# Kernel optimization log

Hardware: AMD Instinct MI355X
Metric: run time of the kernel (lower is better)

## Reference

```python
import jax, jax.numpy as jnp
import numpy as np

IN_DIM = 2048
OUT_DIM = 2048
BASIS_DIM = 64
BATCH = 4
SEQ = 4096
EPS = 1e-5


def _make_bbasis():
    k = np.arange(BASIS_DIM, dtype=np.float64)[:, None]  # (K,1)
    i = np.arange(OUT_DIM, dtype=np.float64)[None, :]    # (1,D)
    return jnp.asarray(np.cos(2.0 * np.pi * (k + 1.0) / (i + 2.0)), dtype=jnp.float32)


def setup_inputs() -> dict:
    key = jax.random.key(0)
    k1, k2, k3, k4 = jax.random.split(key, 4)
    x = jax.random.normal(k1, (BATCH, SEQ, IN_DIM), dtype=jnp.float32)
    # nn.init.uniform_(-0.1, 0.1) style scaling for weights
    W = jax.random.uniform(k2, (OUT_DIM, IN_DIM), dtype=jnp.float32, minval=-0.1, maxval=0.1)
    W_res = jax.random.uniform(k3, (OUT_DIM, IN_DIM), dtype=jnp.float32, minval=-0.1, maxval=0.1)
    Acoeff = jax.random.uniform(k4, (OUT_DIM, BASIS_DIM), dtype=jnp.float32, minval=-0.1, maxval=0.1)
    gamma = jnp.ones((OUT_DIM,), dtype=jnp.float32)
    beta = jnp.zeros((OUT_DIM,), dtype=jnp.float32)
    Bbasis = _make_bbasis()
    return {"x": x, "W": W, "W_res": W_res, "gamma": gamma, "beta": beta,
            "Acoeff": Acoeff, "Bbasis": Bbasis}


def reference(x, W, W_res, gamma, beta, Acoeff, Bbasis):
    # residual projection (use_residual == 'separate')
    residual = jnp.einsum('bsi,oi->bso', x, W_res)          # (B,S,D)
    transformed = jnp.einsum('bsi,oi->bso', x, W)           # (B,S,D)
    # LayerNorm over last dim
    mean = jnp.mean(transformed, axis=-1, keepdims=True)
    var = jnp.mean(jnp.square(transformed - mean), axis=-1, keepdims=True)
    normalized = (transformed - mean) * jax.lax.rsqrt(var + EPS) * gamma + beta
    # periodic basis gather
    seq_len = x.shape[1]
    j = jnp.arange(seq_len) % BASIS_DIM                      # (S,)
    B_vec = Bbasis[j]                                        # (S,D)
    A_vec = Acoeff[:, j].T                                   # (S,D)
    scalars = jnp.einsum('bsd,sd->bs', normalized, B_vec)    # (B,S)
    return scalars[:, :, None] * A_vec[None] + residual      # (B,S,D)
```

## Files before the change

### kernel.cpp

```cpp
#include <hip/hip_runtime.h>
#include <hip/hip_bf16.h>

#define KDIM   2048
#define DDIM   2048
#define MROWS  16384
#define BASIS  64
#define EPSLN  1e-5f
#define NKT    32

typedef __bf16 bf16x8 __attribute__((ext_vector_type(8)));
typedef float  f32x4  __attribute__((ext_vector_type(4)));
typedef unsigned short u16x8 __attribute__((ext_vector_type(8)));

static __device__ __forceinline__ unsigned short f2bf(float f) {
  union { float f; unsigned int u; } v; v.f = f;
  unsigned int r = v.u + 0x7FFFu + ((v.u >> 16) & 1u);
  return (unsigned short)(r >> 16);
}
static __device__ __forceinline__ float bf2f(unsigned short h) {
  union { unsigned int u; float f; } v; v.u = ((unsigned int)h) << 16;
  return v.f;
}

__global__ __launch_bounds__(256) void prep(
    const float* __restrict__ x, const float* __restrict__ W,
    const float* __restrict__ Wres, const float* __restrict__ Ac,
    unsigned short* __restrict__ xbf, unsigned short* __restrict__ Wc,
    float* __restrict__ At) {
  const int b = blockIdx.x, t = threadIdx.x;
  if (b < 2048) {
    const float4* in = (const float4*)x;
    ushort4* op = (ushort4*)xbf;
    const int base = b * 4096;
#pragma unroll
    for (int k = 0; k < 16; ++k) {
      const int i = base + k * 256 + t;
      float4 v = in[i];
      op[i] = make_ushort4(f2bf(v.x), f2bf(v.y), f2bf(v.z), f2bf(v.w));
    }
  } else if (b < 3072) {
    const bool isW = (b < 2560);
    const float4* in = (const float4*)(isW ? W : Wres);
    ushort4* op = (ushort4*)(Wc + (isW ? 0 : 4194304));
    const int base = (isW ? (b - 2048) : (b - 2560)) * 2048;
#pragma unroll
    for (int k = 0; k < 8; ++k) {
      const int i = base + k * 256 + t;
      float4 v = in[i];
      op[i] = make_ushort4(f2bf(v.x), f2bf(v.y), f2bf(v.z), f2bf(v.w));
    }
  } else {
    const int j = b - 3072;
    for (int d = t; d < DDIM; d += 256)
      At[j * DDIM + d] = Ac[d * BASIS + j];
  }
}

__device__ __forceinline__ void gload16(const void* g, void* l) {
  __builtin_amdgcn_global_load_lds(
      (const __attribute__((address_space(1))) unsigned int*)(unsigned long long)g,
      (__attribute__((address_space(3))) unsigned int*)(unsigned int)(unsigned long long)l,
      16, 0, 0);
}
__device__ __forceinline__ void bar() { asm volatile("s_barrier" ::: "memory"); }

__global__ __launch_bounds__(512, 2) void gemm_dual(
    const unsigned short* __restrict__ Abf,
    const unsigned short* __restrict__ Bbf,
    unsigned short* __restrict__ Tout,
    unsigned short* __restrict__ Rout)
{
  __shared__ __align__(16) unsigned short As[2 * 256 * 64];
  __shared__ __align__(16) unsigned short Bs[2 * 256 * 64];

  const int tid  = threadIdx.x;
  const int lane = tid & 63;
  const int wave = tid >> 6;

  const int bid = blockIdx.x;
  const int wg  = (bid & 7) * 128 + (bid >> 3);
  const int bm  = wg >> 4;
  const int bn  = wg & 15;
  const int brow0 = bm * 256;
  const int bcol0 = bn * 256;

  const int srow  = tid >> 3;
  const int sslot = (tid & 7) ^ (srow & 7);
  const unsigned short* pA = Abf + (size_t)(brow0 + srow) * KDIM + sslot * 8;
  const unsigned short* pB = Bbf + (size_t)(bcol0 + srow) * KDIM + sslot * 8;
  const int ldst = wave * 512;

  const int wm   = wave >> 2;
  const int wn   = wave & 3;
  const int frow = lane & 15;
  const int kgrp = lane >> 4;

#define SA(d, kk, c) gload16(pA + (size_t)(c)*64*KDIM + (kk)*64, As + (d)*16384 + (c)*4096 + ldst)
#define SB(d, kk, c) gload16(pB + (size_t)(c)*64*KDIM + (kk)*64, Bs + (d)*16384 + (c)*4096 + ldst)
#define RD_A(mf, kc) (*(const bf16x8*)(Ard + (wm*128 + (mf)*16 + frow)*64 + ((((kc)*4 + kgrp) ^ (frow & 7)) << 3)))
#define RD_B(j, kc)  (*(const bf16x8*)(Brd + (wn*64  + (j)*16  + frow)*64 + ((((kc)*4 + kgrp) ^ (frow & 7)) << 3)))

  f32x4 acc[8][4] = {};

  SA(0,0,0); SA(0,0,1); SA(0,0,2); SA(0,0,3);
  SB(0,0,0); SB(0,0,1); SB(0,0,2); SB(0,0,3);
  SB(1,1,0); SB(1,1,1);
  SA(1,1,0); SA(1,1,2);
  SB(1,1,2); SB(1,1,3);
  asm volatile("s_waitcnt vmcnt(6)" ::: "memory");
  __builtin_amdgcn_sched_barrier(0);
  bar();

  for (int kt = 0; kt < NKT; ++kt) {
    const int d = kt & 1;
    const unsigned short* Ard = As + d * 16384;
    const unsigned short* Brd = Bs + d * 16384;

    bf16x8 bv[4][2], af0[2], af1[2];

#pragma unroll
    for (int j = 0; j < 4; ++j) { bv[j][0] = RD_B(j, 0); bv[j][1] = RD_B(j, 1); }
    af0[0] = RD_A(0, 0); af0[1] = RD_A(0, 1);
    af1[0] = RD_A(1, 0); af1[1] = RD_A(1, 1);
    if (kt < NKT - 1) { SA(d ^ 1, kt + 1, 1); SA(d ^ 1, kt + 1, 3); }
    bar();
    __builtin_amdgcn_s_setprio(1);
#pragma unroll
    for (int j = 0; j < 4; ++j) {
      acc[0][j] = __builtin_amdgcn_mfma_f32_16x16x32_bf16(af0[0], bv[j][0], acc[0][j], 0, 0, 0);
      acc[0][j] = __builtin_amdgcn_mfma_f32_16x16x32_bf16(af0[1], bv[j][1], acc[0][j], 0, 0, 0);
      acc[1][j] = __builtin_amdgcn_mfma_f32_16x16x32_bf16(af1[0], bv[j][0], acc[1][j], 0, 0, 0);
      acc[1][j] = __builtin_amdgcn_mfma_f32_16x16x32_bf16(af1[1], bv[j][1], acc[1][j], 0, 0, 0);
    }
    __builtin_amdgcn_s_setprio(0);
    __builtin_amdgcn_sched_barrier(0);
    bar();

    af0[0] = RD_A(2, 0); af0[1] = RD_A(2, 1);
    af1[0] = RD_A(3, 0); af1[1] = RD_A(3, 1);
    if (kt < NKT - 2) { SB(d, kt + 2, 0); SB(d, kt + 2, 1); }
    bar();
    __builtin_amdgcn_s_setprio(1);
#pragma unroll
    for (int j = 0; j < 4; ++j) {
      acc[2][j] = __builtin_amdgcn_mfma_f32_16x16x32_bf16(af0[0], bv[j][0], acc[2][j], 0, 0, 0);
      acc[2][j] = __builtin_amdgcn_mfma_f32_16x16x32_bf16(af0[1], bv[j][1], acc[2][j], 0, 0, 0);
      acc[3][j] = __builtin_amdgcn_mfma_f32_16x16x32_bf16(af1[0], bv[j][0], acc[3][j], 0, 0, 0);
      acc[3][j] = __builtin_amdgcn_mfma_f32_16x16x32_bf16(af1[1], bv[j][1], acc[3][j], 0, 0, 0);
    }
    __builtin_amdgcn_s_setprio(0);
    __builtin_amdgcn_sched_barrier(0);
    bar();

    af0[0] = RD_A(4, 0); af0[1] = RD_A(4, 1);
    af1[0] = RD_A(5, 0); af1[1] = RD_A(5, 1);
    if (kt < NKT - 2) { SA(d, kt + 2, 0); SA(d, kt + 2, 2); }
    bar();
    __builtin_amdgcn_s_setprio(1);
#pragma unroll
    for (int j = 0; j < 4; ++j) {
      acc[4][j] = __builtin_amdgcn_mfma_f32_16x16x32_bf16(af0[0], bv[j][0], acc[4][j], 0, 0, 0);
      acc[4][j] = __builtin_amdgcn_mfma_f32_16x16x32_bf16(af0[1], bv[j][1], acc[4][j], 0, 0, 0);
      acc[5][j] = __builtin_amdgcn_mfma_f32_16x16x32_bf16(af1[0], bv[j][0], acc[5][j], 0, 0, 0);
      acc[5][j] = __builtin_amdgcn_mfma_f32_16x16x32_bf16(af1[1], bv[j][1], acc[5][j], 0, 0, 0);
    }
    __builtin_amdgcn_s_setprio(0);
    __builtin_amdgcn_sched_barrier(0);
    bar();

    af0[0] = RD_A(6, 0); af0[1] = RD_A(6, 1);
    af1[0] = RD_A(7, 0); af1[1] = RD_A(7, 1);
    if (kt < NKT - 2) { SB(d, kt + 2, 2); SB(d, kt + 2, 3); }
    bar();
    __builtin_amdgcn_s_setprio(1);
#pragma unroll
    for (int j = 0; j < 4; ++j) {
      acc[6][j] = __builtin_amdgcn_mfma_f32_16x16x32_bf16(af0[0], bv[j][0], acc[6][j], 0, 0, 0);
      acc[6][j] = __builtin_amdgcn_mfma_f32_16x16x32_bf16(af0[1], bv[j][1], acc[6][j], 0, 0, 0);
      acc[7][j] = __builtin_amdgcn_mfma_f32_16x16x32_bf16(af1[0], bv[j][0], acc[7][j], 0, 0, 0);
      acc[7][j] = __builtin_amdgcn_mfma_f32_16x16x32_bf16(af1[1], bv[j][1], acc[7][j], 0, 0, 0);
    }
    __builtin_amdgcn_s_setprio(0);
    if (kt < NKT - 2) { asm volatile("s_waitcnt vmcnt(6)" ::: "memory"); }
    else              { asm volatile("s_waitcnt vmcnt(0)" ::: "memory"); }
    __builtin_amdgcn_sched_barrier(0);
    bar();
  }

  unsigned short* Cb = (bn < 8) ? Tout : Rout;
  const int c0 = (bn < 8) ? bcol0 : (bcol0 - 2048);
#pragma unroll
  for (int i = 0; i < 8; ++i) {
    const int r0 = brow0 + wm * 128 + i * 16 + kgrp * 4;
#pragma unroll
    for (int j = 0; j < 4; ++j) {
      const int col = c0 + wn * 64 + j * 16 + frow;
#pragma unroll
      for (int r = 0; r < 4; ++r)
        Cb[(size_t)(r0 + r) * DDIM + col] = f2bf(acc[i][j][r]);
    }
  }
#undef SA
#undef SB
#undef RD_A
#undef RD_B
}

__global__ __launch_bounds__(256) void epilogue(
    const unsigned short* __restrict__ T, const unsigned short* __restrict__ R,
    const float* __restrict__ Bb, const float* __restrict__ At,
    const float* __restrict__ gam, const float* __restrict__ bet,
    float* __restrict__ out)
{
  __shared__ float red[16];
  const int row = blockIdx.x;
  const int s   = row & 4095;
  const int j   = s & 63;
  const int tid = threadIdx.x;
  const size_t rb = (size_t)row * DDIM;
  const int d0 = tid * 8;

  u16x8 tv = *(const u16x8*)(T + rb + d0);
  float t[8];
#pragma unroll
  for (int k = 0; k < 8; ++k) t[k] = bf2f(tv[k]);

  float sum = 0.f, sq = 0.f;
#pragma unroll
  for (int k = 0; k < 8; ++k) { sum += t[k]; sq += t[k] * t[k]; }
#pragma unroll
  for (int off = 32; off > 0; off >>= 1) {
    sum += __shfl_down(sum, off);
    sq  += __shfl_down(sq,  off);
  }
  if ((tid & 63) == 0) { red[tid >> 6] = sum; red[4 + (tid >> 6)] = sq; }
  __syncthreads();
  if (tid == 0) {
    float sAll = red[0] + red[1] + red[2] + red[3];
    float qAll = red[4] + red[5] + red[6] + red[7];
    float m = sAll * (1.0f / 2048.0f);
    float v = qAll * (1.0f / 2048.0f) - m * m;
    red[8] = m;
    red[9] = rsqrtf(v + EPSLN);
  }
  __syncthreads();
  const float mean = red[8], rstd = red[9];

  const size_t jb = (size_t)j * DDIM;
  float4 g0 = *(const float4*)(gam + d0), g1 = *(const float4*)(gam + d0 + 4);
  float4 b0 = *(const float4*)(bet + d0), b1 = *(const float4*)(bet + d0 + 4);
  float4 w0 = *(const float4*)(Bb + jb + d0), w1 = *(const float4*)(Bb + jb + d0 + 4);

  float sc =
      ((t[0] - mean) * rstd * g0.x + b0.x) * w0.x +
      ((t[1] - mean) * rstd * g0.y + b0.y) * w0.y +
      ((t[2] - mean) * rstd * g0.z + b0.z) * w0.z +
      ((t[3] - mean) * rstd * g0.w + b0.w) * w0.w +
      ((t[4] - mean) * rstd * g1.x + b1.x) * w1.x +
      ((t[5] - mean) * rstd * g1.y + b1.y) * w1.y +
      ((t[6] - mean) * rstd * g1.z + b1.z) * w1.z +
      ((t[7] - mean) * rstd * g1.w + b1.w) * w1.w;
#pragma unroll
  for (int off = 32; off > 0; off >>= 1) sc += __shfl_down(sc, off);
  if ((tid & 63) == 0) red[10 + (tid >> 6)] = sc;
  __syncthreads();
  const float scalar = red[10] + red[11] + red[12] + red[13];

  u16x8 rv = *(const u16x8*)(R + rb + d0);
  float4 a0 = *(const float4*)(At + jb + d0), a1 = *(const float4*)(At + jb + d0 + 4);
  float4 o0, o1;
  o0.x = scalar * a0.x + bf2f(rv[0]);  o0.y = scalar * a0.y + bf2f(rv[1]);
  o0.z = scalar * a0.z + bf2f(rv[2]);  o0.w = scalar * a0.w + bf2f(rv[3]);
  o1.x = scalar * a1.x + bf2f(rv[4]);  o1.y = scalar * a1.y + bf2f(rv[5]);
  o1.z = scalar * a1.z + bf2f(rv[6]);  o1.w = scalar * a1.w + bf2f(rv[7]);
  *(float4*)(out + rb + d0)     = o0;
  *(float4*)(out + rb + d0 + 4) = o1;
}

extern "C" void kernel_launch(void* const* d_in, const int* in_sizes, int n_in,
                              void* d_out, int out_size, void* d_ws, size_t ws_size,
                              hipStream_t stream) {
  const float* x      = (const float*)d_in[0];
  const float* W      = (const float*)d_in[1];
  const float* Wres   = (const float*)d_in[2];
  const float* gamma  = (const float*)d_in[3];
  const float* beta   = (const float*)d_in[4];
  const float* Acoeff = (const float*)d_in[5];
  const float* Bbasis = (const float*)d_in[6];
  float* out = (float*)d_out;
  char* ws = (char*)d_ws;

  unsigned short* xbf = (unsigned short*)ws;
  unsigned short* Wc  = (unsigned short*)(ws + 67108864);
  unsigned short* T   = (unsigned short*)(ws + 83886080);
  unsigned short* Rbf = (unsigned short*)(ws + 150994944);
  float* At           = (float*)(ws + 218103808);

  prep<<<3136, 256, 0, stream>>>(x, W, Wres, Acoeff, xbf, Wc, At);

  gemm_dual<<<1024, 512, 0, stream>>>(xbf, Wc, T, Rbf);

  epilogue<<<16384, 256, 0, stream>>>(T, Rbf, Bbasis, At, gamma, beta, out);
}
```

Measured before the change: 538.9 us.

## Restructure epilogue to one row per wave with folded LayerNorm algebra; add lgkm waits

The epilogue now assigns one basis index j per block and processes 16 rows sharing that j, two per wave. The per-column gamma*Bbasis products and their sums, plus the beta·Bbasis sum and the Acoeff row, are precomputed once in registers. Each row then needs a single pass computing sum, sum of squares and the dot product, reduced with wave shuffles only, with no LDS and no __syncthreads. The GEMM main loop also gets explicit lgkmcnt(0) waits before each MFMA cluster. These waits may serialize LDS reads with compute but make the scheduling explicit.

```diff
diff --git a/kernel.cpp b/kernel.cpp
--- a/kernel.cpp
+++ b/kernel.cpp
@@ -63,6 +63,8 @@
       16, 0, 0);
 }
 __device__ __forceinline__ void bar() { asm volatile("s_barrier" ::: "memory"); }
+#define LGKM0 do { asm volatile("s_waitcnt lgkmcnt(0)" ::: "memory"); \
+                   __builtin_amdgcn_sched_barrier(0); } while (0)
 
 __global__ __launch_bounds__(512, 2) void gemm_dual(
     const unsigned short* __restrict__ Abf,
@@ -124,6 +126,7 @@
     af1[0] = RD_A(1, 0); af1[1] = RD_A(1, 1);
     if (kt < NKT - 1) { SA(d ^ 1, kt + 1, 1); SA(d ^ 1, kt + 1, 3); }
     bar();
+    LGKM0;
     __builtin_amdgcn_s_setprio(1);
 #pragma unroll
     for (int j = 0; j < 4; ++j) {
@@ -140,6 +143,7 @@
     af1[0] = RD_A(3, 0); af1[1] = RD_A(3, 1);
     if (kt < NKT - 2) { SB(d, kt + 2, 0); SB(d, kt + 2, 1); }
     bar();
+    LGKM0;
     __builtin_amdgcn_s_setprio(1);
 #pragma unroll
     for (int j = 0; j < 4; ++j) {
@@ -156,6 +160,7 @@
     af1[0] = RD_A(5, 0); af1[1] = RD_A(5, 1);
     if (kt < NKT - 2) { SA(d, kt + 2, 0); SA(d, kt + 2, 2); }
     bar();
+    LGKM0;
     __builtin_amdgcn_s_setprio(1);
 #pragma unroll
     for (int j = 0; j < 4; ++j) {
@@ -172,6 +177,7 @@
     af1[0] = RD_A(7, 0); af1[1] = RD_A(7, 1);
     if (kt < NKT - 2) { SB(d, kt + 2, 2); SB(d, kt + 2, 3); }
     bar();
+    LGKM0;
     __builtin_amdgcn_s_setprio(1);
 #pragma unroll
     for (int j = 0; j < 4; ++j) {
@@ -206,75 +212,76 @@
 #undef RD_B
 }
 
-__global__ __launch_bounds__(256) void epilogue(
+__global__ __launch_bounds__(512) void epilogue(
     const unsigned short* __restrict__ T, const unsigned short* __restrict__ R,
     const float* __restrict__ Bb, const float* __restrict__ At,
     const float* __restrict__ gam, const float* __restrict__ bet,
     float* __restrict__ out)
 {
-  __shared__ float red[16];
-  const int row = blockIdx.x;
-  const int s   = row & 4095;
-  const int j   = s & 63;
-  const int tid = threadIdx.x;
-  const size_t rb = (size_t)row * DDIM;
-  const int d0 = tid * 8;
-
-  u16x8 tv = *(const u16x8*)(T + rb + d0);
-  float t[8];
-#pragma unroll
-  for (int k = 0; k < 8; ++k) t[k] = bf2f(tv[k]);
-
-  float sum = 0.f, sq = 0.f;
-#pragma unroll
-  for (int k = 0; k < 8; ++k) { sum += t[k]; sq += t[k] * t[k]; }
+  const int b   = blockIdx.x;
+  const int j   = b & 63;
+  const int seg = b >> 6;
+  const int wv  = threadIdx.x >> 6;
+  const int l   = threadIdx.x & 63;
+  const size_t jb = (size_t)j * DDIM;
+
+  float4 G[8], A4[8];
+  float sgp = 0.f, sbbp = 0.f;
+#pragma unroll
+  for (int c = 0; c < 8; ++c) {
+    const int col = l * 4 + 256 * c;
+    float4 g = *(const float4*)(gam + col);
+    float4 w = *(const float4*)(Bb + jb + col);
+    float4 be = *(const float4*)(bet + col);
+    A4[c] = *(const float4*)(At + jb + col);
+    G[c].x = g.x * w.x; G[c].y = g.y * w.y; G[c].z = g.z * w.z; G[c].w = g.w * w.w;
+    sgp  += G[c].x + G[c].y + G[c].z + G[c].w;
+    sbbp += be.x * w.x + be.y * w.y + be.z * w.z + be.w * w.w;
+  }
 #pragma unroll
   for (int off = 32; off > 0; off >>= 1) {
-    sum += __shfl_down(sum, off);
-    sq  += __shfl_down(sq,  off);
-  }
-  if ((tid & 63) == 0) { red[tid >> 6] = sum; red[4 + (tid >> 6)] = sq; }
-  __syncthreads();
-  if (tid == 0) {
-    float sAll = red[0] + red[1] + red[2] + red[3];
-    float qAll = red[4] + red[5] + red[6] + red[7];
-    float m = sAll * (1.0f / 2048.0f);
-    float v = qAll * (1.0f / 2048.0f) - m * m;
-    red[8] = m;
-    red[9] = rsqrtf(v + EPSLN);
-  }
-  __syncthreads();
-  const float mean = red[8], rstd = red[9];
-
-  const size_t jb = (size_t)j * DDIM;
-  float4 g0 = *(const float4*)(gam + d0), g1 = *(const float4*)(gam + d0 + 4);
-  float4 b0 = *(const float4*)(bet + d0), b1 = *(const float4*)(bet + d0 + 4);
-  float4 w0 = *(const float4*)(Bb + jb + d0), w1 = *(const float4*)(Bb + jb + d0 + 4);
-
-  float sc =
-      ((t[0] - mean) * rstd * g0.x + b0.x) * w0.x +
-      ((t[1] - mean) * rstd * g0.y + b0.y) * w0.y +
-      ((t[2] - mean) * rstd * g0.z + b0.z) * w0.z +
-      ((t[3] - mean) * rstd * g0.w + b0.w) * w0.w +
-      ((t[4] - mean) * rstd * g1.x + b1.x) * w1.x +
-      ((t[5] - mean) * rstd * g1.y + b1.y) * w1.y +
-      ((t[6] - mean) * rstd * g1.z + b1.z) * w1.z +
-      ((t[7] - mean) * rstd * g1.w + b1.w) * w1.w;
-#pragma unroll
-  for (int off = 32; off > 0; off >>= 1) sc += __shfl_down(sc, off);
-  if ((tid & 63) == 0) red[10 + (tid >> 6)] = sc;
-  __syncthreads();
-  const float scalar = red[10] + red[11] + red[12] + red[13];
-
-  u16x8 rv = *(const u16x8*)(R + rb + d0);
-  float4 a0 = *(const float4*)(At + jb + d0), a1 = *(const float4*)(At + jb + d0 + 4);
-  float4 o0, o1;
-  o0.x = scalar * a0.x + bf2f(rv[0]);  o0.y = scalar * a0.y + bf2f(rv[1]);
-  o0.z = scalar * a0.z + bf2f(rv[2]);  o0.w = scalar * a0.w + bf2f(rv[3]);
-  o1.x = scalar * a1.x + bf2f(rv[4]);  o1.y = scalar * a1.y + bf2f(rv[5]);
-  o1.z = scalar * a1.z + bf2f(rv[6]);  o1.w = scalar * a1.w + bf2f(rv[7]);
-  *(float4*)(out + rb + d0)     = o0;
-  *(float4*)(out + rb + d0 + 4) = o1;
+    sgp  += __shfl_xor(sgp,  off);
+    sbbp += __shfl_xor(sbbp, off);
+  }
+  const float SG = sgp;
+  const float SBB = sbbp;
+
+#pragma unroll
+  for (int rr = 0; rr < 2; ++rr) {
+    const int k = seg * 16 + wv * 2 + rr;
+    const size_t rowb = (size_t)(j + 64 * k) * DDIM;
+    float s1 = 0.f, s2 = 0.f, s3 = 0.f;
+#pragma unroll
+    for (int c = 0; c < 8; ++c) {
+      const int col = l * 4 + 256 * c;
+      ushort4 tv = *(const ushort4*)(T + rowb + col);
+      float t0 = bf2f(tv.x), t1 = bf2f(tv.y), t2 = bf2f(tv.z), t3 = bf2f(tv.w);
+      s1 += t0 + t1 + t2 + t3;
+      s2 += t0 * t0 + t1 * t1 + t2 * t2 + t3 * t3;
+      s3 += t0 * G[c].x + t1 * G[c].y + t2 * G[c].z + t3 * G[c].w;
+    }
+#pragma unroll
+    for (int off = 32; off > 0; off >>= 1) {
+      s1 += __shfl_xor(s1, off);
+      s2 += __shfl_xor(s2, off);
+      s3 += __shfl_xor(s3, off);
+    }
+    const float mean = s1 * (1.0f / 2048.0f);
+    const float var  = s2 * (1.0f / 2048.0f) - mean * mean;
+    const float rstd = rsqrtf(var + EPSLN);
+    const float scalar = rstd * (s3 - mean * SG) + SBB;
+#pragma unroll
+    for (int c = 0; c < 8; ++c) {
+      const int col = l * 4 + 256 * c;
+      ushort4 rv = *(const ushort4*)(R + rowb + col);
+      float4 o;
+      o.x = scalar * A4[c].x + bf2f(rv.x);
+      o.y = scalar * A4[c].y + bf2f(rv.y);
+      o.z = scalar * A4[c].z + bf2f(rv.z);
+      o.w = scalar * A4[c].w + bf2f(rv.w);
+      *(float4*)(out + rowb + col) = o;
+    }
+  }
 }
 
 extern "C" void kernel_launch(void* const* d_in, const int* in_sizes, int n_in,
@@ -300,5 +307,5 @@
 
   gemm_dual<<<1024, 512, 0, stream>>>(xbf, Wc, T, Rbf);
 
-  epilogue<<<16384, 256, 0, stream>>>(T, Rbf, Bbasis, At, gamma, beta, out);
-}
+  epilogue<<<1024, 512, 0, stream>>>(T, Rbf, Bbasis, At, gamma, beta, out);
+}
```

After: 535.4 us. About the same (-0.6%).
